# Optimization experiments

Measured on AMD Instinct MI355X. Metric: run time of the kernel, lower is better.

Reference implementation:

```python
import jax, jax.numpy as jnp
import numpy as np

HEAD_SIZE = 64


def setup_inputs() -> dict:
    key = jax.random.key(0)
    kx, kq, kk, kv = jax.random.split(key, 4)
    B, L, D = 4, 4096, 1024
    scale = 1.0 / np.sqrt(D)
    x = jax.random.normal(kx, (B, L, D), dtype=jnp.float32)
    Wq = jax.random.normal(kq, (D, HEAD_SIZE), dtype=jnp.float32) * scale
    Wk = jax.random.normal(kk, (D, HEAD_SIZE), dtype=jnp.float32) * scale
    Wv = jax.random.normal(kv, (D, HEAD_SIZE), dtype=jnp.float32) * scale
    return {"x": x, "Wq": Wq, "Wk": Wk, "Wv": Wv}


def reference(x, Wq, Wk, Wv):
    B, L, D = x.shape
    H = Wq.shape[1]
    q = jnp.einsum('bld,dh->blh', x, Wq)  # [B,L,H]
    k = jnp.einsum('bld,dh->blh', x, Wk)
    v = jnp.einsum('bld,dh->blh', x, Wv)
    # full L x L score matrix, as in the original module
    scores = jnp.einsum('bqh,bkh->bqk', q, k) / jnp.sqrt(jnp.float32(H))
    causal = jnp.tril(jnp.ones((L, L), dtype=bool))
    scores = jnp.where(causal, scores, -jnp.inf)
    attn = jax.nn.softmax(scores, axis=-1)
    z = jnp.einsum('bqk,bkh->bqh', attn, v)  # [B,L,H]
    return z
```

## Files before the change

kernel.cpp:

```cpp
#include <hip/hip_runtime.h>
#include <stdint.h>

#define L_SEQ 4096
#define D_MODEL 1024
#define HEAD 64
#define CHUNK 512
#define MAXCH 8
#define NQT 32

typedef unsigned short u16;
typedef __attribute__((ext_vector_type(8))) short bf16x8;
typedef __attribute__((ext_vector_type(4))) float f32x4;

static __device__ __forceinline__ u16 f2bf(float f) {
    union { float f; uint32_t u; } c; c.f = f;
    uint32_t u = c.u;
    return (u16)((u + 0x7FFFu + ((u >> 16) & 1u)) >> 16);
}
static __device__ __forceinline__ bf16x8 ld8(const u16* p) { return *(const bf16x8*)p; }

static __device__ __forceinline__ f32x4 mfma16(bf16x8 a, bf16x8 b, f32x4 c) {
    return __builtin_amdgcn_mfma_f32_16x16x32_bf16(a, b, c, 0, 0, 0);
}

static __device__ __forceinline__ void gload16(const u16* g, u16* l) {
    __builtin_amdgcn_global_load_lds(
        (const __attribute__((address_space(1))) void*)g,
        (__attribute__((address_space(3))) void*)l, 16, 0, 0);
}

__global__ __launch_bounds__(256) void conv_w(
    const float* __restrict__ Wq, const float* __restrict__ Wk,
    const float* __restrict__ Wv, u16* __restrict__ Wt)
{
    __shared__ u16 tile[64][72];
    const float* W = (blockIdx.y == 0) ? Wq : (blockIdx.y == 1) ? Wk : Wv;
    u16* dst = Wt + blockIdx.y * (HEAD * D_MODEL);
    const int k0 = blockIdx.x * 64, t = threadIdx.x;
    #pragma unroll
    for (int i = 0; i < 16; i++) {
        int idx = i * 256 + t;
        int kk = idx >> 6, h = idx & 63;
        tile[h][kk] = f2bf(W[(size_t)(k0 + kk) * HEAD + h]);
    }
    __syncthreads();
    #pragma unroll
    for (int i = 0; i < 16; i++) {
        int idx = i * 256 + t;
        int h = idx >> 6, kk = idx & 63;
        dst[(size_t)h * D_MODEL + k0 + kk] = tile[h][kk];
    }
}

__global__ __launch_bounds__(256) void qkv_proj(
    const float* __restrict__ x, const u16* __restrict__ Wt,
    u16* __restrict__ qb, u16* __restrict__ kb, u16* __restrict__ vTb)
{
    __shared__ __align__(16) u16 Wl[2 * 2 * 192 * 32];
    __shared__ __align__(16) u16 Xl[2 * 2 * 32 * 36];
#define WLX(bb,dh,r,c) Wl[(((bb)*2 + (dh))*192 + (r))*32 + (c)]
#define XLX(bb,kh,r,c) Xl[(((bb)*2 + (kh))*32  + (r))*36 + (c)]
#define CT(r,c)        ((u16*)Wl)[(r)*200 + (c)]

    const int t = threadIdx.x;
    const int wv = t >> 6, lane = t & 63;
    const int ln16 = lane & 15, quad = lane >> 4;
    const int w3 = wv * 3;
    const int m0 = blockIdx.x * 32;

    f32x4 acc[2][3] = {};
    float4 xv0, xv1;

    auto issueW = [&](int s, int bb) {
        const int k0 = s * 64;
        #pragma unroll
        for (int k2 = 0; k2 < 6; k2++) {
            int c = wv * 6 + k2;
            int dh = c & 1, g = c >> 1;
            const u16* gp = Wt + (size_t)(g * 16 + (lane >> 2)) * D_MODEL
                               + k0 + dh * 32 + (lane & 3) * 8;
            gload16(gp, &WLX(bb, dh, g * 16 + (lane >> 2), (lane & 3) * 8));
        }
    };
    auto loadx = [&](int s) {
        const int k0 = s * 64;
        int r0 = t >> 4, cs0 = (t & 15) * 4;
        xv0 = *(const float4*)&x[(size_t)(m0 + r0) * D_MODEL + k0 + cs0];
        int idx = 256 + t, r1 = idx >> 4, cs1 = (idx & 15) * 4;
        xv1 = *(const float4*)&x[(size_t)(m0 + r1) * D_MODEL + k0 + cs1];
    };
    auto packx = [&](int bb) {
        int r0 = t >> 4, cs0 = (t & 15) * 4;
        uint2 p0;
        p0.x = (uint32_t)f2bf(xv0.x) | ((uint32_t)f2bf(xv0.y) << 16);
        p0.y = (uint32_t)f2bf(xv0.z) | ((uint32_t)f2bf(xv0.w) << 16);
        *(uint2*)&XLX(bb, cs0 >> 5, r0, cs0 & 31) = p0;
        int idx = 256 + t, r1 = idx >> 4, cs1 = (idx & 15) * 4;
        uint2 p1;
        p1.x = (uint32_t)f2bf(xv1.x) | ((uint32_t)f2bf(xv1.y) << 16);
        p1.y = (uint32_t)f2bf(xv1.z) | ((uint32_t)f2bf(xv1.w) << 16);
        *(uint2*)&XLX(bb, cs1 >> 5, r1, cs1 & 31) = p1;
    };

    issueW(0, 0);
    loadx(0);
    packx(0);
    int buf = 0;
    for (int s = 0; s < 16; s++) {
        __syncthreads();
        if (s + 1 < 16) { issueW(s + 1, buf ^ 1); loadx(s + 1); }
        #pragma unroll
        for (int c = 0; c < 2; c++) {
            bf16x8 xb0 = ld8(&XLX(buf, c, ln16, quad * 8));
            bf16x8 xb1 = ld8(&XLX(buf, c, 16 + ln16, quad * 8));
            #pragma unroll
            for (int j = 0; j < 3; j++) {
                bf16x8 af = ld8(&WLX(buf, c, (w3 + j) * 16 + ln16, quad * 8));
                acc[0][j] = mfma16(af, xb0, acc[0][j]);
                acc[1][j] = mfma16(af, xb1, acc[1][j]);
            }
        }
        if (s + 1 < 16) packx(buf ^ 1);
        buf ^= 1;
    }

    __syncthreads();
    #pragma unroll
    for (int mt = 0; mt < 2; mt++) {
        #pragma unroll
        for (int j = 0; j < 3; j++) {
            int g0 = (w3 + j) * 16 + quad * 4;
            float sc = (g0 < 64) ? 0.125f : 1.0f;
            uint2 pk;
            pk.x = (uint32_t)f2bf(acc[mt][j][0] * sc) | ((uint32_t)f2bf(acc[mt][j][1] * sc) << 16);
            pk.y = (uint32_t)f2bf(acc[mt][j][2] * sc) | ((uint32_t)f2bf(acc[mt][j][3] * sc) << 16);
            *(uint2*)&CT(mt * 16 + ln16, g0) = pk;
        }
    }
    __syncthreads();
    {
        int m = t >> 3, hg = (t & 7) * 8;
        *(bf16x8*)&qb[(size_t)(m0 + m) * HEAD + hg] = *(bf16x8*)&CT(m, hg);
        *(bf16x8*)&kb[(size_t)(m0 + m) * HEAD + hg] = *(bf16x8*)&CT(m, 64 + hg);
        int h = t >> 2, mg = (t & 3) * 8;
        bf16x8 vvv;
        #pragma unroll
        for (int jj = 0; jj < 8; jj++) vvv[jj] = (short)CT(mg + jj, 128 + h);
        int bbt = m0 >> 12, l0 = m0 & 4095;
        *(bf16x8*)&vTb[(size_t)(bbt * HEAD + h) * L_SEQ + l0 + mg] = vvv;
    }
#undef WLX
#undef XLX
#undef CT
}

__global__ __launch_bounds__(256) void attn_chunk(
    const u16* __restrict__ qb, const u16* __restrict__ kb,
    const u16* __restrict__ vT, float* __restrict__ Opart, float* __restrict__ lpart)
{
    const int qt = blockIdx.x, ch = blockIdx.y, b = blockIdx.z;
    if (ch * CHUNK > qt * 128 + 127) return;

    __shared__ __align__(16) u16 Kls[2 * 2 * 64 * 32];
    __shared__ __align__(16) u16 Vls[2 * 2 * 64 * 32];
    __shared__ __align__(16) u16 Pls[4 * 32 * 72];
#define KBX(bb,dh,r,c) Kls[(((bb)*2 + (dh))*64 + (r))*32 + (c)]
#define VBX(bb,kh,r,c) Vls[(((bb)*2 + (kh))*64 + (r))*32 + (c)]
#define PX(r,c)        Pls[((wv)*32 + (r))*72 + (c)]

    const int t = threadIdx.x, wv = t >> 6, lane = t & 63;
    const int ln16 = lane & 15, quad = lane >> 4;
    const int qmin = qt * 128 + wv * 32;

    bf16x8 qf[2][2];
    #pragma unroll
    for (int qn = 0; qn < 2; qn++) {
        const u16* qrp = qb + (size_t)(b * L_SEQ + qmin + qn * 16 + ln16) * HEAD + quad * 8;
        qf[qn][0] = ld8(qrp); qf[qn][1] = ld8(qrp + 32);
    }

    const u16* kbb = kb + (size_t)b * L_SEQ * HEAD;
    const u16* vbb = vT + (size_t)b * HEAD * L_SEQ;

    f32x4 o[2][4] = {};
    float lsum[2] = {0.f, 0.f};

    const int kv_lo = ch * CHUNK;
    const int kv_hi = min(kv_lo + CHUNK, qt * 128 + 128);
    const int nst = (kv_hi - kv_lo) >> 6;

    auto issue_stage = [&](int kv0, int bb) {
        #pragma unroll
        for (int k2 = 0; k2 < 4; k2++) {
            int c = wv * 4 + k2;
            if (c < 8) {
                int dh = c & 1, g = c >> 1;
                const u16* gp = kbb + (size_t)(kv0 + g * 16 + (lane >> 2)) * HEAD
                                    + dh * 32 + (lane & 3) * 8;
                gload16(gp, &KBX(bb, dh, g * 16 + (lane >> 2), (lane & 3) * 8));
            } else {
                int c2 = c - 8, kh = c2 & 1, g = c2 >> 1;
                const u16* gp = vbb + (size_t)(g * 16 + (lane >> 2)) * L_SEQ
                                    + kv0 + kh * 32 + (lane & 3) * 8;
                gload16(gp, &VBX(bb, kh, g * 16 + (lane >> 2), (lane & 3) * 8));
            }
        }
    };

    issue_stage(kv_lo, 0);
    int buf = 0;
    for (int s = 0; s < nst; s++) {
        __syncthreads();
        if (s + 1 < nst) issue_stage(kv_lo + (s + 1) * 64, buf ^ 1);
        const int kv0 = kv_lo + s * 64;

        #pragma unroll
        for (int g = 0; g < 4; g++) {
            bf16x8 ka0 = ld8(&KBX(buf, 0, g * 16 + ln16, quad * 8));
            bf16x8 ka1 = ld8(&KBX(buf, 1, g * 16 + ln16, quad * 8));
            #pragma unroll
            for (int qn = 0; qn < 2; qn++) {
                f32x4 s2 = {};
                s2 = mfma16(ka0, qf[qn][0], s2);
                s2 = mfma16(ka1, qf[qn][1], s2);
                float p0, p1, p2, p3;
                if (kv0 + g * 16 + 15 <= qmin + qn * 16) {
                    p0 = __expf(s2[0]); p1 = __expf(s2[1]);
                    p2 = __expf(s2[2]); p3 = __expf(s2[3]);
                } else {
                    int q = qmin + qn * 16 + ln16;
                    int kv = kv0 + g * 16 + quad * 4;
                    p0 = (kv     <= q) ? __expf(s2[0]) : 0.f;
                    p1 = (kv + 1 <= q) ? __expf(s2[1]) : 0.f;
                    p2 = (kv + 2 <= q) ? __expf(s2[2]) : 0.f;
                    p3 = (kv + 3 <= q) ? __expf(s2[3]) : 0.f;
                }
                lsum[qn] += p0 + p1 + p2 + p3;
                uint2 pk;
                pk.x = (uint32_t)f2bf(p0) | ((uint32_t)f2bf(p1) << 16);
                pk.y = (uint32_t)f2bf(p2) | ((uint32_t)f2bf(p3) << 16);
                *(uint2*)&PX(qn * 16 + ln16, g * 16 + quad * 4) = pk;
            }
        }
        bf16x8 pf[2][2];
        #pragma unroll
        for (int qn = 0; qn < 2; qn++) {
            pf[qn][0] = ld8(&PX(qn * 16 + ln16, quad * 8));
            pf[qn][1] = ld8(&PX(qn * 16 + ln16, 32 + quad * 8));
        }
        #pragma unroll
        for (int hg = 0; hg < 4; hg++) {
            bf16x8 va0 = ld8(&VBX(buf, 0, hg * 16 + ln16, quad * 8));
            bf16x8 va1 = ld8(&VBX(buf, 1, hg * 16 + ln16, quad * 8));
            #pragma unroll
            for (int qn = 0; qn < 2; qn++) {
                o[qn][hg] = mfma16(va0, pf[qn][0], o[qn][hg]);
                o[qn][hg] = mfma16(va1, pf[qn][1], o[qn][hg]);
            }
        }
        buf ^= 1;
    }

    #pragma unroll
    for (int qn = 0; qn < 2; qn++) {
        lsum[qn] += __shfl_xor(lsum[qn], 16);
        lsum[qn] += __shfl_xor(lsum[qn], 32);
    }

    const size_t base = (size_t)((b * NQT + qt) * MAXCH + ch);
    #pragma unroll
    for (int qn = 0; qn < 2; qn++) {
        int q_local = wv * 32 + qn * 16 + ln16;
        #pragma unroll
        for (int hg = 0; hg < 4; hg++)
            *(f32x4*)&Opart[base * 8192 + (size_t)q_local * 64 + hg * 16 + quad * 4] = o[qn][hg];
        if (quad == 0)
            lpart[base * 128 + q_local] = lsum[qn];
    }
#undef KBX
#undef VBX
#undef PX
}

__global__ __launch_bounds__(256) void merge_chunks(
    const float* __restrict__ Opart, const float* __restrict__ lpart,
    float* __restrict__ out)
{
    const int qt = blockIdx.x, b = blockIdx.y;
    const int nch = qt / 4 + 1;
    const int t = threadIdx.x;
    const size_t obase = (size_t)((b * NQT + qt) * MAXCH) * 8192;
    const size_t lbase = (size_t)((b * NQT + qt) * MAXCH) * 128;
    #pragma unroll
    for (int i = 0; i < 8; i++) {
        int idx = i * 256 + t;
        int q = idx >> 4, hg = (idx & 15) * 4;
        f32x4 vals[MAXCH];
        float ls[MAXCH];
        #pragma unroll
        for (int c = 0; c < MAXCH; c++) {
            vals[c] = *(const f32x4*)&Opart[obase + (size_t)c * 8192 + q * 64 + hg];
            ls[c] = lpart[lbase + c * 128 + q];
        }
        float L = 0.f, ax = 0.f, ay = 0.f, az = 0.f, aw = 0.f;
        #pragma unroll
        for (int c = 0; c < MAXCH; c++) {
            float m = (c < nch) ? 1.f : 0.f;
            L += ls[c] * m;
            ax += vals[c][0] * m; ay += vals[c][1] * m;
            az += vals[c][2] * m; aw += vals[c][3] * m;
        }
        float inv = 1.f / L;
        float4 r; r.x = ax * inv; r.y = ay * inv; r.z = az * inv; r.w = aw * inv;
        *(float4*)&out[((size_t)(b * L_SEQ + qt * 128 + q)) * HEAD + hg] = r;
    }
}

extern "C" void kernel_launch(void* const* d_in, const int* in_sizes, int n_in,
                              void* d_out, int out_size, void* d_ws, size_t ws_size,
                              hipStream_t stream) {
    const float* x  = (const float*)d_in[0];
    const float* Wq = (const float*)d_in[1];
    const float* Wk = (const float*)d_in[2];
    const float* Wv = (const float*)d_in[3];
    float* out = (float*)d_out;

    u16* ws16 = (u16*)d_ws;
    u16* Wt  = ws16;
    u16* qb  = Wt + 3 * HEAD * D_MODEL;
    u16* kb  = qb + 16384 * HEAD;
    u16* vTb = kb + 16384 * HEAD;
    float* Opart = (float*)(vTb + 16384 * HEAD);
    float* lpart = Opart + (size_t)1024 * 8192;

    conv_w      <<<dim3(16, 3), 256, 0, stream>>>(Wq, Wk, Wv, Wt);
    qkv_proj    <<<dim3(512), 256, 0, stream>>>(x, Wt, qb, kb, vTb);
    attn_chunk  <<<dim3(NQT, 8, 4), 256, 0, stream>>>(qb, kb, vTb, Opart, lpart);
    merge_chunks<<<dim3(NQT, 4), 256, 0, stream>>>(Opart, lpart, out);
}
```

Baseline: 163.4 us.

## Switch to fp16 MFMA, halve KV chunk size, compact partial buffers, split merge

Result: slower. 167.1 us (+2.3%).

```diff
diff --git a/kernel.cpp b/kernel.cpp
--- a/kernel.cpp
+++ b/kernel.cpp
@@ -4,29 +4,38 @@
 #define L_SEQ 4096
 #define D_MODEL 1024
 #define HEAD 64
-#define CHUNK 512
-#define MAXCH 8
+#define KCH 256
+#define MAXCH 16
 #define NQT 32
 
 typedef unsigned short u16;
-typedef __attribute__((ext_vector_type(8))) short bf16x8;
+typedef _Float16 f16;
+typedef __attribute__((ext_vector_type(8))) f16 f16x8;
+typedef __attribute__((ext_vector_type(2))) __fp16 fp16x2;
 typedef __attribute__((ext_vector_type(4))) float f32x4;
 
-static __device__ __forceinline__ u16 f2bf(float f) {
-    union { float f; uint32_t u; } c; c.f = f;
-    uint32_t u = c.u;
-    return (u16)((u + 0x7FFFu + ((u >> 16) & 1u)) >> 16);
-}
-static __device__ __forceinline__ bf16x8 ld8(const u16* p) { return *(const bf16x8*)p; }
-
-static __device__ __forceinline__ f32x4 mfma16(bf16x8 a, bf16x8 b, f32x4 c) {
-    return __builtin_amdgcn_mfma_f32_16x16x32_bf16(a, b, c, 0, 0, 0);
+static __device__ __forceinline__ u16 f16bits(float f) {
+    union { f16 h; u16 u; } c; c.h = (f16)f; return c.u;
+}
+static __device__ __forceinline__ uint32_t pk16(float a, float b) {
+    union { fp16x2 h; uint32_t u; } c;
+    c.h = __builtin_amdgcn_cvt_pkrtz(a, b);
+    return c.u;
+}
+static __device__ __forceinline__ f16x8 ld8h(const u16* p) { return *(const f16x8*)p; }
+
+static __device__ __forceinline__ f32x4 mfma16h(f16x8 a, f16x8 b, f32x4 c) {
+    return __builtin_amdgcn_mfma_f32_16x16x32_f16(a, b, c, 0, 0, 0);
 }
 
 static __device__ __forceinline__ void gload16(const u16* g, u16* l) {
     __builtin_amdgcn_global_load_lds(
         (const __attribute__((address_space(1))) void*)g,
         (__attribute__((address_space(3))) void*)l, 16, 0, 0);
+}
+
+static __device__ __forceinline__ int Sq(int qt) {
+    return (qt & 1) ? ((qt + 1) * (qt + 1)) >> 2 : (qt * (qt + 2)) >> 2;
 }
 
 __global__ __launch_bounds__(256) void conv_w(
@@ -35,13 +44,14 @@
 {
     __shared__ u16 tile[64][72];
     const float* W = (blockIdx.y == 0) ? Wq : (blockIdx.y == 1) ? Wk : Wv;
+    const float sc = (blockIdx.y == 0) ? 0.18033688f : 1.0f;
     u16* dst = Wt + blockIdx.y * (HEAD * D_MODEL);
     const int k0 = blockIdx.x * 64, t = threadIdx.x;
     #pragma unroll
     for (int i = 0; i < 16; i++) {
         int idx = i * 256 + t;
         int kk = idx >> 6, h = idx & 63;
-        tile[h][kk] = f2bf(W[(size_t)(k0 + kk) * HEAD + h]);
+        tile[h][kk] = f16bits(W[(size_t)(k0 + kk) * HEAD + h] * sc);
     }
     __syncthreads();
     #pragma unroll
@@ -91,35 +101,34 @@
     };
     auto packx = [&](int bb) {
         int r0 = t >> 4, cs0 = (t & 15) * 4;
-        uint2 p0;
-        p0.x = (uint32_t)f2bf(xv0.x) | ((uint32_t)f2bf(xv0.y) << 16);
-        p0.y = (uint32_t)f2bf(xv0.z) | ((uint32_t)f2bf(xv0.w) << 16);
+        uint2 p0; p0.x = pk16(xv0.x, xv0.y); p0.y = pk16(xv0.z, xv0.w);
         *(uint2*)&XLX(bb, cs0 >> 5, r0, cs0 & 31) = p0;
         int idx = 256 + t, r1 = idx >> 4, cs1 = (idx & 15) * 4;
-        uint2 p1;
-        p1.x = (uint32_t)f2bf(xv1.x) | ((uint32_t)f2bf(xv1.y) << 16);
-        p1.y = (uint32_t)f2bf(xv1.z) | ((uint32_t)f2bf(xv1.w) << 16);
+        uint2 p1; p1.x = pk16(xv1.x, xv1.y); p1.y = pk16(xv1.z, xv1.w);
         *(uint2*)&XLX(bb, cs1 >> 5, r1, cs1 & 31) = p1;
     };
 
-    issueW(0, 0);
-    loadx(0);
-    packx(0);
+    loadx(0); issueW(0, 0); packx(0);
     int buf = 0;
     for (int s = 0; s < 16; s++) {
         __syncthreads();
-        if (s + 1 < 16) { issueW(s + 1, buf ^ 1); loadx(s + 1); }
+        f16x8 xb[2][2], af[2][3];
         #pragma unroll
         for (int c = 0; c < 2; c++) {
-            bf16x8 xb0 = ld8(&XLX(buf, c, ln16, quad * 8));
-            bf16x8 xb1 = ld8(&XLX(buf, c, 16 + ln16, quad * 8));
+            xb[c][0] = ld8h(&XLX(buf, c, ln16, quad * 8));
+            xb[c][1] = ld8h(&XLX(buf, c, 16 + ln16, quad * 8));
+            #pragma unroll
+            for (int j = 0; j < 3; j++)
+                af[c][j] = ld8h(&WLX(buf, c, (w3 + j) * 16 + ln16, quad * 8));
+        }
+        if (s + 1 < 16) { loadx(s + 1); issueW(s + 1, buf ^ 1); }
+        #pragma unroll
+        for (int c = 0; c < 2; c++)
             #pragma unroll
             for (int j = 0; j < 3; j++) {
-                bf16x8 af = ld8(&WLX(buf, c, (w3 + j) * 16 + ln16, quad * 8));
-                acc[0][j] = mfma16(af, xb0, acc[0][j]);
-                acc[1][j] = mfma16(af, xb1, acc[1][j]);
-            }
-        }
+                acc[0][j] = mfma16h(af[c][j], xb[c][0], acc[0][j]);
+                acc[1][j] = mfma16h(af[c][j], xb[c][1], acc[1][j]);
+            }
         if (s + 1 < 16) packx(buf ^ 1);
         buf ^= 1;
     }
@@ -130,53 +139,53 @@
         #pragma unroll
         for (int j = 0; j < 3; j++) {
             int g0 = (w3 + j) * 16 + quad * 4;
-            float sc = (g0 < 64) ? 0.125f : 1.0f;
             uint2 pk;
-            pk.x = (uint32_t)f2bf(acc[mt][j][0] * sc) | ((uint32_t)f2bf(acc[mt][j][1] * sc) << 16);
-            pk.y = (uint32_t)f2bf(acc[mt][j][2] * sc) | ((uint32_t)f2bf(acc[mt][j][3] * sc) << 16);
+            pk.x = pk16(acc[mt][j][0], acc[mt][j][1]);
+            pk.y = pk16(acc[mt][j][2], acc[mt][j][3]);
             *(uint2*)&CT(mt * 16 + ln16, g0) = pk;
         }
     }
     __syncthreads();
     {
         int m = t >> 3, hg = (t & 7) * 8;
-        *(bf16x8*)&qb[(size_t)(m0 + m) * HEAD + hg] = *(bf16x8*)&CT(m, hg);
-        *(bf16x8*)&kb[(size_t)(m0 + m) * HEAD + hg] = *(bf16x8*)&CT(m, 64 + hg);
+        *(f16x8*)&qb[(size_t)(m0 + m) * HEAD + hg] = *(f16x8*)&CT(m, hg);
+        *(f16x8*)&kb[(size_t)(m0 + m) * HEAD + hg] = *(f16x8*)&CT(m, 64 + hg);
         int h = t >> 2, mg = (t & 3) * 8;
-        bf16x8 vvv;
-        #pragma unroll
-        for (int jj = 0; jj < 8; jj++) vvv[jj] = (short)CT(mg + jj, 128 + h);
+        f16x8 vvv;
+        #pragma unroll
+        for (int jj = 0; jj < 8; jj++)
+            ((u16*)&vvv)[jj] = CT(mg + jj, 128 + h);
         int bbt = m0 >> 12, l0 = m0 & 4095;
-        *(bf16x8*)&vTb[(size_t)(bbt * HEAD + h) * L_SEQ + l0 + mg] = vvv;
+        *(f16x8*)&vTb[(size_t)(bbt * HEAD + h) * L_SEQ + l0 + mg] = vvv;
     }
 #undef WLX
 #undef XLX
 #undef CT
 }
 
-__global__ __launch_bounds__(256) void attn_chunk(
+__global__ __launch_bounds__(256, 4) void attn_chunk(
     const u16* __restrict__ qb, const u16* __restrict__ kb,
     const u16* __restrict__ vT, float* __restrict__ Opart, float* __restrict__ lpart)
 {
     const int qt = blockIdx.x, ch = blockIdx.y, b = blockIdx.z;
-    if (ch * CHUNK > qt * 128 + 127) return;
-
-    __shared__ __align__(16) u16 Kls[2 * 2 * 64 * 32];
-    __shared__ __align__(16) u16 Vls[2 * 2 * 64 * 32];
+    if (ch * KCH > qt * 128 + 127) return;
+
+    __shared__ __align__(16) u16 Kls[2 * 64 * 32];
+    __shared__ __align__(16) u16 Vls[2 * 64 * 32];
     __shared__ __align__(16) u16 Pls[4 * 32 * 72];
-#define KBX(bb,dh,r,c) Kls[(((bb)*2 + (dh))*64 + (r))*32 + (c)]
-#define VBX(bb,kh,r,c) Vls[(((bb)*2 + (kh))*64 + (r))*32 + (c)]
-#define PX(r,c)        Pls[((wv)*32 + (r))*72 + (c)]
+#define KBX(dh,r,c) Kls[((dh)*64 + (r))*32 + (c)]
+#define VBX(kh,r,c) Vls[((kh)*64 + (r))*32 + (c)]
+#define PX(r,c)     Pls[((wv)*32 + (r))*72 + (c)]
 
     const int t = threadIdx.x, wv = t >> 6, lane = t & 63;
     const int ln16 = lane & 15, quad = lane >> 4;
     const int qmin = qt * 128 + wv * 32;
 
-    bf16x8 qf[2][2];
+    f16x8 qf[2][2];
     #pragma unroll
     for (int qn = 0; qn < 2; qn++) {
         const u16* qrp = qb + (size_t)(b * L_SEQ + qmin + qn * 16 + ln16) * HEAD + quad * 8;
-        qf[qn][0] = ld8(qrp); qf[qn][1] = ld8(qrp + 32);
+        qf[qn][0] = ld8h(qrp); qf[qn][1] = ld8h(qrp + 32);
     }
 
     const u16* kbb = kb + (size_t)b * L_SEQ * HEAD;
@@ -185,11 +194,11 @@
     f32x4 o[2][4] = {};
     float lsum[2] = {0.f, 0.f};
 
-    const int kv_lo = ch * CHUNK;
-    const int kv_hi = min(kv_lo + CHUNK, qt * 128 + 128);
+    const int kv_lo = ch * KCH;
+    const int kv_hi = min(kv_lo + KCH, qt * 128 + 128);
     const int nst = (kv_hi - kv_lo) >> 6;
 
-    auto issue_stage = [&](int kv0, int bb) {
+    auto issue_stage = [&](int kv0) {
         #pragma unroll
         for (int k2 = 0; k2 < 4; k2++) {
             int c = wv * 4 + k2;
@@ -197,68 +206,66 @@
                 int dh = c & 1, g = c >> 1;
                 const u16* gp = kbb + (size_t)(kv0 + g * 16 + (lane >> 2)) * HEAD
                                     + dh * 32 + (lane & 3) * 8;
-                gload16(gp, &KBX(bb, dh, g * 16 + (lane >> 2), (lane & 3) * 8));
+                gload16(gp, &KBX(dh, g * 16 + (lane >> 2), (lane & 3) * 8));
             } else {
                 int c2 = c - 8, kh = c2 & 1, g = c2 >> 1;
                 const u16* gp = vbb + (size_t)(g * 16 + (lane >> 2)) * L_SEQ
                                     + kv0 + kh * 32 + (lane & 3) * 8;
-                gload16(gp, &VBX(bb, kh, g * 16 + (lane >> 2), (lane & 3) * 8));
+                gload16(gp, &VBX(kh, g * 16 + (lane >> 2), (lane & 3) * 8));
             }
         }
     };
 
-    issue_stage(kv_lo, 0);
-    int buf = 0;
     for (int s = 0; s < nst; s++) {
+        const int kv0 = kv_lo + s * 64;
+        issue_stage(kv0);
         __syncthreads();
-        if (s + 1 < nst) issue_stage(kv_lo + (s + 1) * 64, buf ^ 1);
-        const int kv0 = kv_lo + s * 64;
 
         #pragma unroll
         for (int g = 0; g < 4; g++) {
-            bf16x8 ka0 = ld8(&KBX(buf, 0, g * 16 + ln16, quad * 8));
-            bf16x8 ka1 = ld8(&KBX(buf, 1, g * 16 + ln16, quad * 8));
+            f16x8 ka0 = ld8h(&KBX(0, g * 16 + ln16, quad * 8));
+            f16x8 ka1 = ld8h(&KBX(1, g * 16 + ln16, quad * 8));
             #pragma unroll
             for (int qn = 0; qn < 2; qn++) {
                 f32x4 s2 = {};
-                s2 = mfma16(ka0, qf[qn][0], s2);
-                s2 = mfma16(ka1, qf[qn][1], s2);
+                s2 = mfma16h(ka0, qf[qn][0], s2);
+                s2 = mfma16h(ka1, qf[qn][1], s2);
                 float p0, p1, p2, p3;
                 if (kv0 + g * 16 + 15 <= qmin + qn * 16) {
-                    p0 = __expf(s2[0]); p1 = __expf(s2[1]);
-                    p2 = __expf(s2[2]); p3 = __expf(s2[3]);
+                    p0 = __builtin_amdgcn_exp2f(s2[0]);
+                    p1 = __builtin_amdgcn_exp2f(s2[1]);
+                    p2 = __builtin_amdgcn_exp2f(s2[2]);
+                    p3 = __builtin_amdgcn_exp2f(s2[3]);
                 } else {
                     int q = qmin + qn * 16 + ln16;
                     int kv = kv0 + g * 16 + quad * 4;
-                    p0 = (kv     <= q) ? __expf(s2[0]) : 0.f;
-                    p1 = (kv + 1 <= q) ? __expf(s2[1]) : 0.f;
-                    p2 = (kv + 2 <= q) ? __expf(s2[2]) : 0.f;
-                    p3 = (kv + 3 <= q) ? __expf(s2[3]) : 0.f;
+                    p0 = (kv     <= q) ? __builtin_amdgcn_exp2f(s2[0]) : 0.f;
+                    p1 = (kv + 1 <= q) ? __builtin_amdgcn_exp2f(s2[1]) : 0.f;
+                    p2 = (kv + 2 <= q) ? __builtin_amdgcn_exp2f(s2[2]) : 0.f;
+                    p3 = (kv + 3 <= q) ? __builtin_amdgcn_exp2f(s2[3]) : 0.f;
                 }
-                lsum[qn] += p0 + p1 + p2 + p3;
-                uint2 pk;
-                pk.x = (uint32_t)f2bf(p0) | ((uint32_t)f2bf(p1) << 16);
-                pk.y = (uint32_t)f2bf(p2) | ((uint32_t)f2bf(p3) << 16);
+                lsum[qn] += (p0 + p1) + (p2 + p3);
+                uint2 pk; pk.x = pk16(p0, p1); pk.y = pk16(p2, p3);
                 *(uint2*)&PX(qn * 16 + ln16, g * 16 + quad * 4) = pk;
             }
         }
-        bf16x8 pf[2][2];
+        f16x8 pf[2][2];
         #pragma unroll
         for (int qn = 0; qn < 2; qn++) {
-            pf[qn][0] = ld8(&PX(qn * 16 + ln16, quad * 8));
-            pf[qn][1] = ld8(&PX(qn * 16 + ln16, 32 + quad * 8));
+            pf[qn][0] = ld8h(&PX(qn * 16 + ln16, quad * 8));
+            pf[qn][1] = ld8h(&PX(qn * 16 + ln16, 32 + quad * 8));
         }
         #pragma unroll
         for (int hg = 0; hg < 4; hg++) {
-            bf16x8 va0 = ld8(&VBX(buf, 0, hg * 16 + ln16, quad * 8));
-            bf16x8 va1 = ld8(&VBX(buf, 1, hg * 16 + ln16, quad * 8));
+            f16x8 va0 = ld8h(&VBX(0, hg * 16 + ln16, quad * 8));
+            f16x8 va1 = ld8h(&VBX(1, hg * 16 + ln16, quad * 8));
             #pragma unroll
             for (int qn = 0; qn < 2; qn++) {
-                o[qn][hg] = mfma16(va0, pf[qn][0], o[qn][hg]);
-                o[qn][hg] = mfma16(va1, pf[qn][1], o[qn][hg]);
-            }
-        }
-        buf ^= 1;
+                o[qn][hg] = mfma16h(va0, pf[qn][0], o[qn][hg]);
+                o[qn][hg] = mfma16h(va1, pf[qn][1], o[qn][hg]);
+            }
+        }
+        __syncthreads();
     }
 
     #pragma unroll
@@ -267,7 +274,7 @@
         lsum[qn] += __shfl_xor(lsum[qn], 32);
     }
 
-    const size_t base = (size_t)((b * NQT + qt) * MAXCH + ch);
+    const size_t base = (size_t)(b * 272 + Sq(qt) + ch);
     #pragma unroll
     for (int qn = 0; qn < 2; qn++) {
         int q_local = wv * 32 + qn * 16 + ln16;
@@ -286,29 +293,23 @@
     const float* __restrict__ Opart, const float* __restrict__ lpart,
     float* __restrict__ out)
 {
-    const int qt = blockIdx.x, b = blockIdx.y;
-    const int nch = qt / 4 + 1;
+    const int qt = blockIdx.x, qseg = blockIdx.y, b = blockIdx.z;
+    const int nch = (qt + 2) >> 1;
     const int t = threadIdx.x;
-    const size_t obase = (size_t)((b * NQT + qt) * MAXCH) * 8192;
-    const size_t lbase = (size_t)((b * NQT + qt) * MAXCH) * 128;
-    #pragma unroll
-    for (int i = 0; i < 8; i++) {
+    const size_t obase = (size_t)(b * 272 + Sq(qt)) * 8192;
+    const size_t lbase = (size_t)(b * 272 + Sq(qt)) * 128;
+    #pragma unroll
+    for (int i = 0; i < 2; i++) {
         int idx = i * 256 + t;
-        int q = idx >> 4, hg = (idx & 15) * 4;
-        f32x4 vals[MAXCH];
-        float ls[MAXCH];
+        int q = qseg * 32 + (idx >> 4), hg = (idx & 15) * 4;
+        float L = 0.f, ax = 0.f, ay = 0.f, az = 0.f, aw = 0.f;
         #pragma unroll
         for (int c = 0; c < MAXCH; c++) {
-            vals[c] = *(const f32x4*)&Opart[obase + (size_t)c * 8192 + q * 64 + hg];
-            ls[c] = lpart[lbase + c * 128 + q];
-        }
-        float L = 0.f, ax = 0.f, ay = 0.f, az = 0.f, aw = 0.f;
-        #pragma unroll
-        for (int c = 0; c < MAXCH; c++) {
-            float m = (c < nch) ? 1.f : 0.f;
-            L += ls[c] * m;
-            ax += vals[c][0] * m; ay += vals[c][1] * m;
-            az += vals[c][2] * m; aw += vals[c][3] * m;
+            if (c < nch) {
+                L += lpart[lbase + c * 128 + q];
+                const float4 v = *(const float4*)&Opart[obase + (size_t)c * 8192 + q * 64 + hg];
+                ax += v.x; ay += v.y; az += v.z; aw += v.w;
+            }
         }
         float inv = 1.f / L;
         float4 r; r.x = ax * inv; r.y = ay * inv; r.z = az * inv; r.w = aw * inv;
@@ -331,10 +332,10 @@
     u16* kb  = qb + 16384 * HEAD;
     u16* vTb = kb + 16384 * HEAD;
     float* Opart = (float*)(vTb + 16384 * HEAD);
-    float* lpart = Opart + (size_t)1024 * 8192;
+    float* lpart = Opart + (size_t)4 * 272 * 8192;
 
     conv_w      <<<dim3(16, 3), 256, 0, stream>>>(Wq, Wk, Wv, Wt);
     qkv_proj    <<<dim3(512), 256, 0, stream>>>(x, Wt, qb, kb, vTb);
-    attn_chunk  <<<dim3(NQT, 8, 4), 256, 0, stream>>>(qb, kb, vTb, Opart, lpart);
-    merge_chunks<<<dim3(NQT, 4), 256, 0, stream>>>(Opart, lpart, out);
-}
+    attn_chunk  <<<dim3(NQT, MAXCH, 4), 256, 0, stream>>>(qb, kb, vTb, Opart, lpart);
+    merge_chunks<<<dim3(NQT, 4, 4), 256, 0, stream>>>(Opart, lpart, out);
+}
```
